# Performance work log

Measured on AMD Instinct MI355X. Metric: run time of the kernel, lower is better.

The kernel has to match this reference:

```python
import math
import jax, jax.numpy as jnp
import numpy as np

EMB = 1024
HEADS = 16
HEAD_DIM = EMB // HEADS


def setup_inputs() -> dict:
    key = jax.random.key(0)
    ks = jax.random.split(key, 6)
    b, l = 4, 4096
    x = jax.random.normal(ks[0], (b, l, EMB), dtype=jnp.float32)
    # torch Linear weight shape (out, in); xavier_normal std = sqrt(2/(in+out))
    std = math.sqrt(2.0 / (EMB + EMB))
    Wq = jax.random.normal(ks[1], (EMB, EMB), dtype=jnp.float32) * std
    Wk = jax.random.normal(ks[2], (EMB, EMB), dtype=jnp.float32) * std
    Wv = jax.random.normal(ks[3], (EMB, EMB), dtype=jnp.float32) * std
    Wu = jax.random.normal(ks[4], (EMB, EMB), dtype=jnp.float32) * std
    Wo = jax.random.normal(ks[5], (EMB, EMB), dtype=jnp.float32) * std
    return {"x": x, "Wq": Wq, "Wk": Wk, "Wv": Wv, "Wu": Wu, "Wo": Wo}


def _srms_norm(x, eps=1e-12):
    # SRMSNorm over last dim with scale 1/sqrt(head_dims), computed in fp32
    dtype = x.dtype
    xf = x.astype(jnp.float32)
    scale = 1.0 / math.sqrt(x.shape[-1])
    n = jnp.linalg.norm(xf * scale, axis=-1, keepdims=True)
    return (xf / jnp.maximum(n, eps)).astype(dtype)


def reference(x, Wq, Wk, Wv, Wu, Wo):
    b, l, d = x.shape
    h, hd = HEADS, HEAD_DIM
    scale = math.sqrt(hd)

    def proj(W):
        return jnp.einsum('bld,ed->ble', x, W).reshape(b, l, h, hd).transpose(0, 2, 1, 3)

    q = jax.nn.relu(proj(Wq)) / scale        # (b,h,l,hd)
    k = jax.nn.relu(proj(Wk)) / scale
    v = proj(Wv)
    u = jax.nn.silu(proj(Wu))

    kv = jnp.einsum('bhlk,bhlv->bhkv', k, v)  # (b,h,hd,hd) state
    out = jnp.einsum('bhlk,bhkv->bhlv', q, kv)
    out = _srms_norm(out) * u
    out = out.transpose(0, 2, 1, 3).reshape(b, l, d)
    return jnp.einsum('bld,ed->ble', out, Wo)
```

## Files before the change

kernel.cpp:

```cpp
#include <hip/hip_runtime.h>

typedef _Float16 f16;
typedef _Float16 f16x4 __attribute__((ext_vector_type(4)));
typedef _Float16 f16x8 __attribute__((ext_vector_type(8)));
typedef float f32x4 __attribute__((ext_vector_type(4)));

#define EMB 1024
#define SEQL 4096
#define BATCH 4
#define NH 16
#define HD 64
#define BH 64
#define MROWS 16384
#define KVSPLIT 16

#define GLOAD_LDS(gp, lp) \
    __builtin_amdgcn_global_load_lds((const __attribute__((address_space(1))) void*)(gp), \
                                     (__attribute__((address_space(3))) void*)(lp), 16, 0, 0)

__global__ void cvt_kernel(const float* __restrict__ in, f16* __restrict__ out, int n4) {
    int i = blockIdx.x * blockDim.x + threadIdx.x;
    if (i < n4) {
        float4 v = ((const float4*)in)[i];
        f16x4 o = { (f16)v.x, (f16)v.y, (f16)v.z, (f16)v.w };
        ((f16x4*)out)[i] = o;
    }
}

struct WPtrs { const float* p[5]; };

__global__ void cvt_w_kernel(WPtrs wp, f16* __restrict__ out) {
    int i = blockIdx.x * blockDim.x + threadIdx.x;
    int wsel = blockIdx.y;
    const float4* src = (const float4*)wp.p[wsel];
    float4 v = src[i];
    f16x4 o = { (f16)v.x, (f16)v.y, (f16)v.z, (f16)v.w };
    ((f16x4*)(out + (size_t)wsel * EMB * EMB))[i] = o;
}

__global__ void zero_kernel(float4* __restrict__ p, int n4) {
    int i = blockIdx.x * blockDim.x + threadIdx.x;
    if (i < n4) p[i] = float4{0.f, 0.f, 0.f, 0.f};
}


#define FENCE asm volatile("" ::: "memory")
#define WAITV(N) asm volatile("s_waitcnt vmcnt(" #N ")" ::: "memory")
#define BAR do { FENCE; __builtin_amdgcn_s_barrier(); FENCE; } while (0)

template<int MODE>
__global__ __launch_bounds__(512, 2) void gemm_kernel(
    const f16* __restrict__ A, const f16* __restrict__ Bt,
    void* __restrict__ Cv, int M, int N, int K)
{
    __shared__ f16 As[2][256 * 64];
    __shared__ f16 Bs[2][256 * 64];

    const int tid  = threadIdx.x;
    const int lane = tid & 63;
    const int w    = tid >> 6;
    const int rw   = lane & 15;
    const int quad = lane >> 4;
    const int wm   = w >> 2;
    const int wn   = w & 3;
    const int m0 = blockIdx.y * 256;
    const int n0 = blockIdx.x * 256;
    const size_t Ks = (size_t)K;
    const int NT = K >> 6;

    const int srow8 = lane >> 3;
    const int slog  = (lane & 7) ^ srow8;
    const f16* gA = A  + (size_t)(m0 + w * 8 + srow8) * Ks + slog * 8;
    const f16* gB = Bt + (size_t)(n0 + w * 8 + srow8) * Ks + slog * 8;
    const int lst = w * 512;

#define STAGE_A(H, T, BUF) do { \
    GLOAD_LDS(gA + (size_t)((H) * 128 +  0) * Ks + (T) * 64, &As[BUF][(H) * 8192 + lst]); \
    GLOAD_LDS(gA + (size_t)((H) * 128 + 64) * Ks + (T) * 64, &As[BUF][(H) * 8192 + 4096 + lst]); \
} while (0)
#define STAGE_B(H, T, BUF) do { \
    GLOAD_LDS(gB + (size_t)((H) * 128 +  0) * Ks + (T) * 64, &Bs[BUF][(H) * 8192 + lst]); \
    GLOAD_LDS(gB + (size_t)((H) * 128 + 64) * Ks + (T) * 64, &Bs[BUF][(H) * 8192 + 4096 + lst]); \
} while (0)

    const int rw7   = rw & 7;
    const int s0o   = ( quad      ^ rw7) * 8;
    const int s1o   = ((quad + 4) ^ rw7) * 8;
    const int abase = (wm * 64 + rw) * 64;
    const int bbase = (wn * 32 + rw) * 64;

    f32x4 acc[2][2][4][2] = {};
    f16x8 af[4][2], bf[2][2];

#define READ_A(QM, BUF) do { \
    _Pragma("unroll") \
    for (int mi = 0; mi < 4; ++mi) { \
        af[mi][0] = *(const f16x8*)&As[BUF][(QM) * 8192 + abase + mi * 1024 + s0o]; \
        af[mi][1] = *(const f16x8*)&As[BUF][(QM) * 8192 + abase + mi * 1024 + s1o]; \
    } \
} while (0)
#define READ_B(QN, BUF) do { \
    _Pragma("unroll") \
    for (int nj = 0; nj < 2; ++nj) { \
        bf[nj][0] = *(const f16x8*)&Bs[BUF][(QN) * 8192 + bbase + nj * 1024 + s0o]; \
        bf[nj][1] = *(const f16x8*)&Bs[BUF][(QN) * 8192 + bbase + nj * 1024 + s1o]; \
    } \
} while (0)
#define MFMA_Q(QM, QN) do { \
    __builtin_amdgcn_s_setprio(1); \
    _Pragma("unroll") \
    for (int mi = 0; mi < 4; ++mi) \
        _Pragma("unroll") \
        for (int nj = 0; nj < 2; ++nj) { \
            acc[QM][QN][mi][nj] = __builtin_amdgcn_mfma_f32_16x16x32_f16(bf[nj][0], af[mi][0], acc[QM][QN][mi][nj], 0, 0, 0); \
            acc[QM][QN][mi][nj] = __builtin_amdgcn_mfma_f32_16x16x32_f16(bf[nj][1], af[mi][1], acc[QM][QN][mi][nj], 0, 0, 0); \
        } \
    __builtin_amdgcn_s_setprio(0); \
} while (0)

    STAGE_A(0, 0, 0);
    STAGE_B(0, 0, 0);
    STAGE_B(1, 0, 0);
    STAGE_A(1, 0, 0);
    if (NT > 1) { STAGE_A(0, 1, 1); WAITV(2); } else { WAITV(0); }
    BAR;

    for (int kt = 0; kt < NT; ++kt) {
        const int cur = kt & 1, nxt = cur ^ 1;
        const bool p1 = (kt + 1 < NT), p2 = (kt + 2 < NT);
        READ_A(0, cur); READ_B(0, cur);
        if (p1) { STAGE_B(0, kt + 1, nxt); WAITV(6); } else { WAITV(2); }
        BAR; MFMA_Q(0, 0); BAR;
        READ_B(1, cur);
        if (p1) { STAGE_B(1, kt + 1, nxt); WAITV(6); } else { WAITV(0); }
        BAR; MFMA_Q(0, 1); BAR;
        READ_A(1, cur);
        if (p1) { STAGE_A(1, kt + 1, nxt); WAITV(6); } else { WAITV(0); }
        BAR; MFMA_Q(1, 1); BAR;
        READ_B(0, cur);
        if (p2) { STAGE_A(0, kt + 2, cur); WAITV(6); } else { WAITV(4); }
        BAR; MFMA_Q(1, 0); BAR;
    }

    #pragma unroll
    for (int qm = 0; qm < 2; ++qm)
    #pragma unroll
    for (int qn = 0; qn < 2; ++qn)
    #pragma unroll
    for (int mi = 0; mi < 4; ++mi)
    #pragma unroll
    for (int nj = 0; nj < 2; ++nj) {
        const int m_idx = m0 + qm * 128 + wm * 64 + mi * 16 + rw;
        const int n_idx = n0 + qn * 128 + wn * 32 + nj * 16 + quad * 4;
        f32x4 a = acc[qm][qn][mi][nj];
        if (MODE == 0) {
            float4 vv = { a[0], a[1], a[2], a[3] };
            *(float4*)&((float*)Cv)[(size_t)m_idx * N + n_idx] = vv;
        } else if (MODE == 3) {
            int sel = n_idx >> 10, e = n_idx & 1023;
            int b = m_idx >> 12, l = m_idx & 4095, h = e >> 6, hdi = e & 63;
            f16x4 o;
            #pragma unroll
            for (int r = 0; r < 4; r++) {
                float v = a[r];
                o[r] = (f16)(sel ? (v / (1.0f + __expf(-v))) : (fmaxf(v, 0.0f) * 0.125f));
            }
            *(f16x4*)&((f16*)Cv)[(size_t)sel * MROWS * EMB +
                                 (((size_t)(b * 16 + h) * 4096 + l) << 6) + hdi] = o;
        } else {
            int sel = m_idx >> 10, e = m_idx & 1023;
            int b = n_idx >> 12, l = n_idx & 4095;
            f16x4 o;
            #pragma unroll
            for (int r = 0; r < 4; r++) {
                float v = a[r];
                o[r] = (f16)(sel ? v : (fmaxf(v, 0.0f) * 0.125f));
            }
            *(f16x4*)&((f16*)Cv)[(size_t)sel * MROWS * EMB +
                                 (((size_t)b * 1024 + e) << 12) + l] = o;
        }
    }
#undef STAGE_A
#undef STAGE_B
#undef READ_A
#undef READ_B
#undef MFMA_Q
}

__global__ __launch_bounds__(256) void kv_split_kernel(
    const f16* __restrict__ kT, const f16* __restrict__ vT, float* __restrict__ kv32)
{
    const int bh    = blockIdx.x;
    const int chunk = blockIdx.y;
    const int lane  = threadIdx.x & 63;
    const int w     = threadIdx.x >> 6;
    const int rw    = lane & 15;
    const int quad  = lane >> 4;
    const int lbase = chunk * (SEQL / KVSPLIT);

    const f16* kp = kT + (size_t)bh * HD * SEQL + (size_t)(w * 16 + rw) * SEQL + lbase + quad * 8;
    const f16* vp = vT + (size_t)bh * HD * SEQL + (size_t)rw * SEQL + lbase + quad * 8;

    f32x4 acc[4] = {};
    for (int k0 = 0; k0 < SEQL / KVSPLIT; k0 += 32) {
        f16x8 a = *(const f16x8*)(kp + k0);
        #pragma unroll
        for (int t = 0; t < 4; t++) {
            f16x8 b = *(const f16x8*)(vp + (size_t)16 * t * SEQL + k0);
            acc[t] = __builtin_amdgcn_mfma_f32_16x16x32_f16(a, b, acc[t], 0, 0, 0);
        }
    }
    float* out = kv32 + (size_t)bh * HD * HD;
    #pragma unroll
    for (int t = 0; t < 4; t++)
        #pragma unroll
        for (int r = 0; r < 4; r++)
            atomicAdd(&out[(w * 16 + quad * 4 + r) * 64 + t * 16 + rw], acc[t][r]);
}

__global__ __launch_bounds__(256) void ret_out_kernel(
    const f16* __restrict__ q, const f16* __restrict__ u,
    const float* __restrict__ kv32, f16* __restrict__ o)
{
    const int bh    = blockIdx.x;
    const int chunk = blockIdx.y;
    const int lane  = threadIdx.x & 63;
    const int w     = threadIdx.x >> 6;
    const int rw    = lane & 15;
    const int quad  = lane >> 4;

    const float* kvp = kv32 + (size_t)bh * 4096;
    f16x8 bf[2][4];
    #pragma unroll
    for (int s = 0; s < 2; s++)
        #pragma unroll
        for (int t = 0; t < 4; t++)
            #pragma unroll
            for (int j = 0; j < 8; j++)
                bf[s][t][j] = (f16)kvp[(s * 32 + quad * 8 + j) * 64 + t * 16 + rw];

    const f16* qp = q + (size_t)bh * SEQL * HD;
    const f16* up = u + (size_t)bh * SEQL * HD;
    const int b = bh >> 4, h = bh & 15;
    f16* op = o + (size_t)b * SEQL * EMB + h * 64;

    const int l_wave = chunk * 512 + w * 128;
    for (int s = 0; s < 8; s++) {
        const int l0 = l_wave + s * 16;
        f16x8 a0 = *(const f16x8*)(qp + (size_t)(l0 + rw) * 64 + quad * 8);
        f16x8 a1 = *(const f16x8*)(qp + (size_t)(l0 + rw) * 64 + 32 + quad * 8);
        f32x4 acc[4] = {};
        #pragma unroll
        for (int t = 0; t < 4; t++) {
            acc[t] = __builtin_amdgcn_mfma_f32_16x16x32_f16(a0, bf[0][t], acc[t], 0, 0, 0);
            acc[t] = __builtin_amdgcn_mfma_f32_16x16x32_f16(a1, bf[1][t], acc[t], 0, 0, 0);
        }
        float inv[4];
        #pragma unroll
        for (int r = 0; r < 4; r++) {
            float ss = acc[0][r] * acc[0][r] + acc[1][r] * acc[1][r]
                     + acc[2][r] * acc[2][r] + acc[3][r] * acc[3][r];
            #pragma unroll
            for (int msk = 1; msk < 16; msk <<= 1)
                ss += __shfl_xor(ss, msk, 16);
            inv[r] = 8.0f / fmaxf(sqrtf(ss), 8e-12f);
        }
        #pragma unroll
        for (int t = 0; t < 4; t++)
            #pragma unroll
            for (int r = 0; r < 4; r++) {
                int l = l0 + quad * 4 + r;
                int col = t * 16 + rw;
                float uval = (float)up[(size_t)l * 64 + col];
                op[(size_t)l * EMB + col] = (f16)(acc[t][r] * inv[r] * uval);
            }
    }
}

extern "C" void kernel_launch(void* const* d_in, const int* in_sizes, int n_in,
                              void* d_out, int out_size, void* d_ws, size_t ws_size,
                              hipStream_t stream)
{
    const float* x = (const float*)d_in[0];
    WPtrs wp;
    wp.p[0] = (const float*)d_in[1];
    wp.p[1] = (const float*)d_in[4];
    wp.p[2] = (const float*)d_in[2];
    wp.p[3] = (const float*)d_in[3];
    wp.p[4] = (const float*)d_in[5];

    char* ws = (char*)d_ws;
    size_t off = 0;
    f16* x16 = (f16*)(ws + off); off += (size_t)MROWS * EMB * 2;
    f16* w16 = (f16*)(ws + off); off += (size_t)5 * EMB * EMB * 2;
    f16* qb  = (f16*)(ws + off); off += (size_t)MROWS * EMB * 2;
    f16* ub  = (f16*)(ws + off); off += (size_t)MROWS * EMB * 2;
    f16* kTb = (f16*)(ws + off); off += (size_t)MROWS * EMB * 2;
    f16* vTb = (f16*)(ws + off); off += (size_t)MROWS * EMB * 2;
    float* kv32 = (float*)(ws + off); off += (size_t)BH * HD * HD * 4;
    f16* ob  = x16;
    (void)ub; (void)vTb;

    cvt_kernel<<<(MROWS * EMB / 4) / 256, 256, 0, stream>>>(x, x16, MROWS * EMB / 4);
    cvt_w_kernel<<<dim3((EMB * EMB / 4) / 256, 5), 256, 0, stream>>>(wp, w16);
    zero_kernel<<<(BH * HD * HD / 4 + 255) / 256, 256, 0, stream>>>((float4*)kv32, BH * HD * HD / 4);

    f16* Wqu = w16;
    f16* Wkv = w16 + (size_t)2 * EMB * EMB;
    f16* Wo  = w16 + (size_t)4 * EMB * EMB;

    dim3 blk(512);
    gemm_kernel<3><<<dim3(8, 64), blk, 0, stream>>>(x16, Wqu, qb, MROWS, 2 * EMB, EMB);
    gemm_kernel<4><<<dim3(64, 8), blk, 0, stream>>>(Wkv, x16, kTb, 2 * EMB, MROWS, EMB);

    kv_split_kernel<<<dim3(BH, KVSPLIT), dim3(256), 0, stream>>>(kTb, vTb, kv32);
    ret_out_kernel<<<dim3(BH, 8), dim3(256), 0, stream>>>(qb, ub, kv32, ob);

    gemm_kernel<0><<<dim3(4, 64), blk, 0, stream>>>(ob, Wo, d_out, MROWS, EMB, EMB);
}
```

Baseline: 395.0 us.

## Double-register B fragments and drop barriers in GEMM main loop

```diff
diff --git a/kernel.cpp b/kernel.cpp
--- a/kernel.cpp
+++ b/kernel.cpp
@@ -90,30 +90,30 @@
     const int bbase = (wn * 32 + rw) * 64;
 
     f32x4 acc[2][2][4][2] = {};
-    f16x8 af[4][2], bf[2][2];
-
-#define READ_A(QM, BUF) do { \
+    f16x8 af[4][2], bf0[2][2], bf1[2][2];
+
+#define READ_AF(QM, BUF) do { \
     _Pragma("unroll") \
     for (int mi = 0; mi < 4; ++mi) { \
         af[mi][0] = *(const f16x8*)&As[BUF][(QM) * 8192 + abase + mi * 1024 + s0o]; \
         af[mi][1] = *(const f16x8*)&As[BUF][(QM) * 8192 + abase + mi * 1024 + s1o]; \
     } \
 } while (0)
-#define READ_B(QN, BUF) do { \
+#define READ_BF(DST, QN, BUF) do { \
     _Pragma("unroll") \
     for (int nj = 0; nj < 2; ++nj) { \
-        bf[nj][0] = *(const f16x8*)&Bs[BUF][(QN) * 8192 + bbase + nj * 1024 + s0o]; \
-        bf[nj][1] = *(const f16x8*)&Bs[BUF][(QN) * 8192 + bbase + nj * 1024 + s1o]; \
+        DST[nj][0] = *(const f16x8*)&Bs[BUF][(QN) * 8192 + bbase + nj * 1024 + s0o]; \
+        DST[nj][1] = *(const f16x8*)&Bs[BUF][(QN) * 8192 + bbase + nj * 1024 + s1o]; \
     } \
 } while (0)
-#define MFMA_Q(QM, QN) do { \
+#define MFMA_Q(QM, QN, BF) do { \
     __builtin_amdgcn_s_setprio(1); \
     _Pragma("unroll") \
     for (int mi = 0; mi < 4; ++mi) \
         _Pragma("unroll") \
         for (int nj = 0; nj < 2; ++nj) { \
-            acc[QM][QN][mi][nj] = __builtin_amdgcn_mfma_f32_16x16x32_f16(bf[nj][0], af[mi][0], acc[QM][QN][mi][nj], 0, 0, 0); \
-            acc[QM][QN][mi][nj] = __builtin_amdgcn_mfma_f32_16x16x32_f16(bf[nj][1], af[mi][1], acc[QM][QN][mi][nj], 0, 0, 0); \
+            acc[QM][QN][mi][nj] = __builtin_amdgcn_mfma_f32_16x16x32_f16(BF[nj][0], af[mi][0], acc[QM][QN][mi][nj], 0, 0, 0); \
+            acc[QM][QN][mi][nj] = __builtin_amdgcn_mfma_f32_16x16x32_f16(BF[nj][1], af[mi][1], acc[QM][QN][mi][nj], 0, 0, 0); \
         } \
     __builtin_amdgcn_s_setprio(0); \
 } while (0)
@@ -128,18 +128,24 @@
     for (int kt = 0; kt < NT; ++kt) {
         const int cur = kt & 1, nxt = cur ^ 1;
         const bool p1 = (kt + 1 < NT), p2 = (kt + 2 < NT);
-        READ_A(0, cur); READ_B(0, cur);
-        if (p1) { STAGE_B(0, kt + 1, nxt); WAITV(6); } else { WAITV(2); }
-        BAR; MFMA_Q(0, 0); BAR;
-        READ_B(1, cur);
-        if (p1) { STAGE_B(1, kt + 1, nxt); WAITV(6); } else { WAITV(0); }
-        BAR; MFMA_Q(0, 1); BAR;
-        READ_A(1, cur);
-        if (p1) { STAGE_A(1, kt + 1, nxt); WAITV(6); } else { WAITV(0); }
-        BAR; MFMA_Q(1, 1); BAR;
-        READ_B(0, cur);
-        if (p2) { STAGE_A(0, kt + 2, cur); WAITV(6); } else { WAITV(4); }
-        BAR; MFMA_Q(1, 0); BAR;
+        if (p1) STAGE_B(0, kt + 1, nxt);
+        READ_AF(0, cur);
+        READ_BF(bf0, 0, cur);
+        if (p1) { WAITV(6); } else { WAITV(2); }
+        BAR;
+        MFMA_Q(0, 0, bf0);
+        if (p1) STAGE_B(1, kt + 1, nxt);
+        READ_BF(bf1, 1, cur);
+        if (p1) { WAITV(6); } else { WAITV(0); }
+        BAR;
+        MFMA_Q(0, 1, bf1);
+        if (p1) STAGE_A(1, kt + 1, nxt);
+        READ_AF(1, cur);
+        MFMA_Q(1, 1, bf1);
+        if (p2) STAGE_A(0, kt + 2, cur);
+        if (p2) { WAITV(6); } else if (p1) { WAITV(4); } else { WAITV(0); }
+        BAR;
+        MFMA_Q(1, 0, bf0);
     }
 
     #pragma unroll
@@ -182,8 +188,8 @@
     }
 #undef STAGE_A
 #undef STAGE_B
-#undef READ_A
-#undef READ_B
+#undef READ_AF
+#undef READ_BF
 #undef MFMA_Q
 }
 
```

Result: slower. 430.3 us (+8.9%).

## Fuse prep kernels and merge QU/KV projection GEMMs into one launch

Applied to the files above, without the earlier changes.

```diff
diff --git a/kernel.cpp b/kernel.cpp
--- a/kernel.cpp
+++ b/kernel.cpp
@@ -18,29 +18,33 @@
     __builtin_amdgcn_global_load_lds((const __attribute__((address_space(1))) void*)(gp), \
                                      (__attribute__((address_space(3))) void*)(lp), 16, 0, 0)
 
-__global__ void cvt_kernel(const float* __restrict__ in, f16* __restrict__ out, int n4) {
-    int i = blockIdx.x * blockDim.x + threadIdx.x;
-    if (i < n4) {
-        float4 v = ((const float4*)in)[i];
+struct WPtrs { const float* p[5]; };
+
+#define NXB (MROWS * EMB / 4 / 256)
+#define NWB (5 * EMB * EMB / 4 / 256)
+#define NZB (BH * HD * HD / 4 / 256)
+__global__ void prep_kernel(const float* __restrict__ x, WPtrs wp,
+                            f16* __restrict__ x16, f16* __restrict__ w16,
+                            float4* __restrict__ kvz)
+{
+    int gid = blockIdx.x;
+    int t = threadIdx.x;
+    if (gid < NXB) {
+        int i = gid * 256 + t;
+        float4 v = ((const float4*)x)[i];
         f16x4 o = { (f16)v.x, (f16)v.y, (f16)v.z, (f16)v.w };
-        ((f16x4*)out)[i] = o;
-    }
-}
-
-struct WPtrs { const float* p[5]; };
-
-__global__ void cvt_w_kernel(WPtrs wp, f16* __restrict__ out) {
-    int i = blockIdx.x * blockDim.x + threadIdx.x;
-    int wsel = blockIdx.y;
-    const float4* src = (const float4*)wp.p[wsel];
-    float4 v = src[i];
-    f16x4 o = { (f16)v.x, (f16)v.y, (f16)v.z, (f16)v.w };
-    ((f16x4*)(out + (size_t)wsel * EMB * EMB))[i] = o;
-}
-
-__global__ void zero_kernel(float4* __restrict__ p, int n4) {
-    int i = blockIdx.x * blockDim.x + threadIdx.x;
-    if (i < n4) p[i] = float4{0.f, 0.f, 0.f, 0.f};
+        ((f16x4*)x16)[i] = o;
+    } else if (gid < NXB + NWB) {
+        int i = (gid - NXB) * 256 + t;
+        int wsel = i >> 18;
+        int j = i & 262143;
+        float4 v = ((const float4*)wp.p[wsel])[j];
+        f16x4 o = { (f16)v.x, (f16)v.y, (f16)v.z, (f16)v.w };
+        ((f16x4*)(w16 + (size_t)wsel * EMB * EMB))[j] = o;
+    } else {
+        int i = (gid - NXB - NWB) * 256 + t;
+        kvz[i] = float4{0.f, 0.f, 0.f, 0.f};
+    }
 }
 
 
@@ -63,15 +67,34 @@
     const int quad = lane >> 4;
     const int wm   = w >> 2;
     const int wn   = w & 3;
-    const int m0 = blockIdx.y * 256;
-    const int n0 = blockIdx.x * 256;
+
+    const f16* Ap = A;
+    const f16* Bp = Bt;
+    char* Cp = (char*)Cv;
+    bool sel_qu = true;
+    int m0, n0;
+    if (MODE == 34) {
+        int bid = blockIdx.x;
+        if (bid < 512) {
+            m0 = (bid >> 3) * 256; n0 = (bid & 7) * 256;
+        } else {
+            bid -= 512;
+            m0 = (bid >> 6) * 256; n0 = (bid & 63) * 256;
+            Ap = Bt + (size_t)2 * EMB * EMB;
+            Bp = A;
+            Cp = (char*)Cv + (size_t)2 * MROWS * EMB * 2;
+            sel_qu = false;
+        }
+    } else {
+        m0 = blockIdx.y * 256; n0 = blockIdx.x * 256;
+    }
     const size_t Ks = (size_t)K;
     const int NT = K >> 6;
 
     const int srow8 = lane >> 3;
     const int slog  = (lane & 7) ^ srow8;
-    const f16* gA = A  + (size_t)(m0 + w * 8 + srow8) * Ks + slog * 8;
-    const f16* gB = Bt + (size_t)(n0 + w * 8 + srow8) * Ks + slog * 8;
+    const f16* gA = Ap + (size_t)(m0 + w * 8 + srow8) * Ks + slog * 8;
+    const f16* gB = Bp + (size_t)(n0 + w * 8 + srow8) * Ks + slog * 8;
     const int lst = w * 512;
 
 #define STAGE_A(H, T, BUF) do { \
@@ -156,7 +179,7 @@
         if (MODE == 0) {
             float4 vv = { a[0], a[1], a[2], a[3] };
             *(float4*)&((float*)Cv)[(size_t)m_idx * N + n_idx] = vv;
-        } else if (MODE == 3) {
+        } else if (sel_qu) {
             int sel = n_idx >> 10, e = n_idx & 1023;
             int b = m_idx >> 12, l = m_idx & 4095, h = e >> 6, hdi = e & 63;
             f16x4 o;
@@ -165,7 +188,7 @@
                 float v = a[r];
                 o[r] = (f16)(sel ? (v / (1.0f + __expf(-v))) : (fmaxf(v, 0.0f) * 0.125f));
             }
-            *(f16x4*)&((f16*)Cv)[(size_t)sel * MROWS * EMB +
+            *(f16x4*)&((f16*)Cp)[(size_t)sel * MROWS * EMB +
                                  (((size_t)(b * 16 + h) * 4096 + l) << 6) + hdi] = o;
         } else {
             int sel = m_idx >> 10, e = m_idx & 1023;
@@ -176,7 +199,7 @@
                 float v = a[r];
                 o[r] = (f16)(sel ? v : (fmaxf(v, 0.0f) * 0.125f));
             }
-            *(f16x4*)&((f16*)Cv)[(size_t)sel * MROWS * EMB +
+            *(f16x4*)&((f16*)Cp)[(size_t)sel * MROWS * EMB +
                                  (((size_t)b * 1024 + e) << 12) + l] = o;
         }
     }
@@ -301,20 +324,14 @@
     f16* ob  = x16;
     (void)ub; (void)vTb;
 
-    cvt_kernel<<<(MROWS * EMB / 4) / 256, 256, 0, stream>>>(x, x16, MROWS * EMB / 4);
-    cvt_w_kernel<<<dim3((EMB * EMB / 4) / 256, 5), 256, 0, stream>>>(wp, w16);
-    zero_kernel<<<(BH * HD * HD / 4 + 255) / 256, 256, 0, stream>>>((float4*)kv32, BH * HD * HD / 4);
-
-    f16* Wqu = w16;
-    f16* Wkv = w16 + (size_t)2 * EMB * EMB;
-    f16* Wo  = w16 + (size_t)4 * EMB * EMB;
-
-    dim3 blk(512);
-    gemm_kernel<3><<<dim3(8, 64), blk, 0, stream>>>(x16, Wqu, qb, MROWS, 2 * EMB, EMB);
-    gemm_kernel<4><<<dim3(64, 8), blk, 0, stream>>>(Wkv, x16, kTb, 2 * EMB, MROWS, EMB);
+    prep_kernel<<<NXB + NWB + NZB, 256, 0, stream>>>(x, wp, x16, w16, (float4*)kv32);
+
+    f16* Wo = w16 + (size_t)4 * EMB * EMB;
+
+    gemm_kernel<34><<<1024, 512, 0, stream>>>(x16, w16, qb, MROWS, 2 * EMB, EMB);
 
     kv_split_kernel<<<dim3(BH, KVSPLIT), dim3(256), 0, stream>>>(kTb, vTb, kv32);
     ret_out_kernel<<<dim3(BH, 8), dim3(256), 0, stream>>>(qb, ub, kv32, ob);
 
-    gemm_kernel<0><<<dim3(4, 64), blk, 0, stream>>>(ob, Wo, d_out, MROWS, EMB, EMB);
-}
+    gemm_kernel<0><<<dim3(4, 64), dim3(512), 0, stream>>>(ob, Wo, d_out, MROWS, EMB, EMB);
+}
```

Result: faster. 381.9 us (-3.3%).
